# Optimization experiments

Hardware: AMD Instinct MI355X
Metric: run time of the kernel (lower is better)

## Reference

```python
import jax, jax.numpy as jnp
import numpy as np

B = 256        # graphs per batch
NPG = 256      # nodes per graph (uniform -> to_dense_batch is a reshape, mask = ones)
NTOT = B * NPG
E = 1_048_576
F_IN = 64
HID = 128
HEADS = 5
K1, K2 = 32, 8
MEMH = 100
NCLS = 12
TAU = 1.0
EPS = 1e-8


def setup_inputs() -> dict:
    key = jax.random.key(0)
    ks = jax.random.split(key, 24)
    f32 = jnp.float32
    def nrm(k, shape, s=0.05):
        return jax.random.normal(k, shape, f32) * s
    inp = {
        "x": jax.random.normal(ks[0], (NTOT, F_IN), f32),
        "edge_index": jax.random.randint(ks[1], (2, E), 0, NTOT, jnp.int32),
        "batch": jnp.repeat(jnp.arange(B, dtype=jnp.int32), NPG),
        # GraphConv q0 (num_feats -> hidden): lin_rel (bias) + lin_root (no bias)
        "W_rel0": nrm(ks[2], (F_IN, HID)), "b_rel0": jnp.zeros((HID,), f32),
        "W_root0": nrm(ks[3], (F_IN, HID)),
        # GraphConv q1 (hidden -> hidden)
        "W_rel1": nrm(ks[4], (HID, HID)), "b_rel1": jnp.zeros((HID,), f32),
        "W_root1": nrm(ks[5], (HID, HID)),
        # BatchNorm1d affine params
        "bn_gamma": jnp.ones((HID,), f32), "bn_beta": jnp.zeros((HID,), f32),
        # MemConv layer 0: keys ~ U[0,1) as torch.rand, conv1x1 [heads], lin F->MEMH
        "keys0": jax.random.uniform(ks[6], (HEADS, K1, HID), f32),
        "convw0": nrm(ks[7], (HEADS,), 0.2),
        "lin_W0": nrm(ks[8], (HID, MEMH)), "lin_b0": jnp.zeros((MEMH,), f32),
        # MemConv layer 1 (num_features = mem_hidden_dim)
        "keys1": jax.random.uniform(ks[9], (HEADS, K2, MEMH), f32),
        "convw1": nrm(ks[10], (HEADS,), 0.2),
        "lin_W1": nrm(ks[11], (MEMH, MEMH)), "lin_b1": jnp.zeros((MEMH,), f32),
        # MLP head
        "mlp_W1": nrm(ks[12], (MEMH, 50)), "mlp_b1": jnp.zeros((50,), f32),
        "mlp_W2": nrm(ks[13], (50, NCLS)), "mlp_b2": jnp.zeros((NCLS,), f32),
    }
    return inp


def _graph_conv(x, src, dst, W_rel, b_rel, W_root):
    # PyG GraphConv, aggr='add': out_i = lin_rel(sum_{j in N(i)} x_j) + lin_root(x_i)
    msg = x[src]                                            # [E, F] gather
    aggr = jax.ops.segment_sum(msg, dst, num_segments=NTOT)  # [N, F] scatter-add
    return aggr @ W_rel + b_rel + x @ W_root


def _kl_reg(C):
    P = C ** 2
    cn = C.sum(axis=-2, keepdims=True) + EPS
    P = P / cn
    pn = P.sum(axis=-1, keepdims=True) + EPS
    P = P / pn
    return 100.0 * (P * (jnp.log(P + EPS) - jnp.log(C + EPS))).sum()


def _mem_conv(Q, keys, conv_w, lin_W, lin_b, mask):
    # Q: [B, N, F]; keys: [H, K, F]; mask: [B, N] or None
    # pairwise L2 distance via norm expansion (same math as the broadcast-diff)
    qsq = (Q * Q).sum(-1)                                   # [B, N]
    ksq = (keys * keys).sum(-1)                             # [H, K]
    qk = jnp.einsum('bnf,hkf->bhnk', Q, keys)               # [B, H, N, K]
    d2 = qsq[:, None, :, None] + ksq[None, :, None, :] - 2.0 * qk
    C = jnp.sqrt(jnp.maximum(d2, 1e-12))
    if mask is not None:
        ext = mask[:, None, :, None]                        # [B,1,N,1]
        C = C * ext
    # gmn kernel: student-t style normalization over keys
    C = (1.0 + C * C / TAU) ** (-(0.5 * TAU + 0.5))
    C = C / C.sum(axis=-1, keepdims=True)
    if mask is not None:
        C = C * ext
    # conv1x1 over heads (no bias) then squeeze head dim
    C = jnp.einsum('h,bhnk->bnk', conv_w, C)
    C = jax.nn.softmax(C, axis=-1)                          # [B, N, K]
    if mask is not None:
        C = C * mask[:, :, None]
    kl = _kl_reg(C)
    V = jnp.einsum('bnk,bnf->bkf', C, Q)                    # [B, K, F]
    out = jax.nn.leaky_relu(V @ lin_W + lin_b)              # slope 0.01 (torch default)
    return out, kl


def reference(x, edge_index, batch, W_rel0, b_rel0, W_root0, W_rel1, b_rel1,
              W_root1, bn_gamma, bn_beta, keys0, convw0, lin_W0, lin_b0,
              keys1, convw1, lin_W1, lin_b1, mlp_W1, mlp_b1, mlp_W2, mlp_b2):
    src, dst = edge_index[0], edge_index[1]
    q = jax.nn.relu(_graph_conv(x, src, dst, W_rel0, b_rel0, W_root0))
    q = jax.nn.relu(_graph_conv(q, src, dst, W_rel1, b_rel1, W_root1))
    # BatchNorm1d over all (padded-)node rows, training stats, eps=1e-5
    mu = q.mean(axis=0)
    var = ((q - mu) ** 2).mean(axis=0)
    q = (q - mu) * jax.lax.rsqrt(var + 1e-5) * bn_gamma + bn_beta
    Q = q.reshape(B, NPG, HID)                              # to_dense_batch (uniform graphs)
    mask = jnp.ones((B, NPG), jnp.float32)
    q1, kl1 = _mem_conv(Q, keys0, convw0, lin_W0, lin_b0, mask)
    q2, kl2 = _mem_conv(q1, keys1, convw1, lin_W1, lin_b1, None)
    h = q2.mean(axis=-2)                                    # [B, MEMH]
    yh = jax.nn.leaky_relu(h @ mlp_W1 + mlp_b1) @ mlp_W2 + mlp_b2
    return yh, (kl1 + kl2) / NTOT
```

## Files before the change

kernel.cpp:

```cpp
#include <hip/hip_runtime.h>
#include <hip/hip_bf16.h>

#define NTOT   65536
#define NEDGE  1048576
#define HEADS  5
#define K1     32
#define K2     8
#define MEMH   100
#define EPSF   1e-8f

#define OFF_DEG     0x0000000
#define OFF_CURSOR  0x0040000
#define OFF_WT1     0x0040000
#define OFF_WT2     0x0050000
#define OFF_OFFS    0x0080000
#define OFF_BNSUM   0x00C0000
#define OFF_BNSQ    0x00C0400
#define OFF_SCALE   0x00C0800
#define OFF_SHIFT   0x00C0A00
#define OFF_KSQ0    0x00C0C00
#define OFF_KSQ1    0x00C0E80
#define OFF_KL      0x00C0F40
#define OFF_FLAG    0x00C0F60
#define OFF_W       0x00C1000
#define OFF_K0B     0x0128000
#define OFF_CN      0x0134000
#define OFF_BH      0x013C000
#define OFF_EBASE   0x013C400
#define OFF_BCUR    0x013C800
#define OFF_CSR     0x0140000
#define OFF_A       0x0540000
#define OFF_AH128   0x0540000
#define OFF_AL128   0x1540000
#define OFF_AH64    0x0540000
#define OFF_AL64    0x0D40000
#define OFF_B       0x2540000
#define OFF_EBUF    0x2540000
#define OFF_QH      0x2540000
#define OFF_QL      0x3540000
#define OFF_C       0x4540000
#define OFF_XH      0x4540000
#define OFF_XL      0x4D40000
#define OFF_CG      0x4540000
#define OFF_V       0x4D40000
#define OFF_MQ1     0x5140000
#define OFF_MQ2     0x5460000

#define W_WREL0  0
#define W_BREL0  8192
#define W_WROOT0 8320
#define W_WREL1  16512
#define W_BREL1  32896
#define W_WROOT1 33024
#define W_GAMMA  49408
#define W_BETA   49536
#define W_KEYS0  49664
#define W_CONVW0 70144
#define W_LINW0  70149
#define W_LINB0  82949
#define W_KEYS1  83049
#define W_CONVW1 87049
#define W_LINW1  87054
#define W_LINB1  97054
#define W_MLPW1  97154
#define W_MLPB1  102154
#define W_MLPW2  102204
#define W_MLPB2  102804
#define W_TOTAL  102816

typedef __attribute__((ext_vector_type(8))) short  bf16x8;
typedef __attribute__((ext_vector_type(4))) float  f32x4;

__device__ __forceinline__ float bf2f(unsigned short u){
  union { unsigned int i; float f; } v; v.i = ((unsigned int)u) << 16; return v.f;
}
__device__ __forceinline__ unsigned short f2bf(float f){
  union { float f; unsigned int i; } v; v.f = f;
  unsigned int r = (v.i + 0x7FFFu + ((v.i >> 16) & 1u)) >> 16;
  return (unsigned short)r;
}

__device__ const int g_seg[21] = {0,8192,8320,16512,32896,33024,49408,49536,49664,
                                  70144,70149,82949,83049,87049,87054,97054,97154,
                                  102154,102204,102804,102816};
struct WPtrs { const void* p[20]; };

__global__ void k_detect(const unsigned short* __restrict__ xr, int* flag){
  int t = threadIdx.x & 63;
  unsigned short u = xr[2*t];
  int e = (u >> 7) & 0xFF;
  bool plaus = (u != 0) && (e >= 115) && (e <= 135);
  unsigned long long m = __ballot(plaus);
  if(t == 0) flag[0] = (__popcll(m) >= 48) ? 1 : 0;
}

__global__ __launch_bounds__(256) void k_cvtx(const void* __restrict__ xin,
                                              const int* __restrict__ flag,
                                              unsigned short* __restrict__ xH,
                                              unsigned short* __restrict__ xL){
  int i = blockIdx.x*256 + threadIdx.x;
  float v;
  if(flag[0]) v = bf2f(((const unsigned short*)xin)[i]);
  else        v = ((const float*)xin)[i];
  unsigned short h = f2bf(v);
  xH[i] = h;
  xL[i] = f2bf(v - bf2f(h));
}

__global__ __launch_bounds__(256) void k_cvtw(WPtrs wp, const int* __restrict__ flag,
                                              float* __restrict__ wout){
  int i = blockIdx.x*256 + threadIdx.x;
  if(i >= W_TOTAL) return;
  int s = 0;
  #pragma unroll
  for(int k=0;k<20;k++) if(i >= g_seg[k+1]) s = k+1;
  int j = i - g_seg[s];
  const void* src = wp.p[s];
  wout[i] = flag[0] ? bf2f(((const unsigned short*)src)[j]) : ((const float*)src)[j];
}

__global__ __launch_bounds__(256) void k_cvtaux(const float* __restrict__ W,
                                                unsigned short* __restrict__ k0b,
                                                unsigned short* __restrict__ wt1,
                                                unsigned short* __restrict__ wt2){
  int i = blockIdx.x*256 + threadIdx.x;
  if(i < HEADS*K1*128) k0b[i] = f2bf(W[W_KEYS0 + i]);
  if(i < 128*64){
    int col = i>>6, k = i&63;
    float wr = W[W_WREL0  + k*128 + col];
    float wo = W[W_WROOT0 + k*128 + col];
    unsigned short rh = f2bf(wr), oh = f2bf(wo);
    wt1[i]         = rh;
    wt1[ 8192 + i] = f2bf(wr - bf2f(rh));
    wt1[16384 + i] = oh;
    wt1[24576 + i] = f2bf(wo - bf2f(oh));
  }
  if(i < 128*128){
    int col = i>>7, k = i&127;
    float wr = W[W_WREL1  + k*128 + col];
    float wo = W[W_WROOT1 + k*128 + col];
    unsigned short rh = f2bf(wr), oh = f2bf(wo);
    wt2[i]         = rh;
    wt2[16384 + i] = f2bf(wr - bf2f(rh));
    wt2[32768 + i] = oh;
    wt2[49152 + i] = f2bf(wo - bf2f(oh));
  }
}

__global__ __launch_bounds__(256) void k_init(unsigned long long* bnsum,
                                              unsigned long long* bnsq, float* kl, float* cn,
                                              int* bhist){
  int i = blockIdx.x*256 + threadIdx.x;
  if(i < 128){ bnsum[i]=0ULL; bnsq[i]=0ULL; }
  if(i < 2) kl[i]=0.f;
  if(i < 256*32) cn[i]=0.f;
  if(i < 256) bhist[i]=0;
}

__global__ __launch_bounds__(256) void k_bin1(const int* __restrict__ dst, int* bhist){
  __shared__ int hist[256];
  const int t = threadIdx.x;
  hist[t] = 0; __syncthreads();
  const int e0 = blockIdx.x*4096 + t;
  #pragma unroll 4
  for(int j=0;j<16;j++) atomicAdd(&hist[dst[e0 + j*256] >> 8], 1);
  __syncthreads();
  if(hist[t]) atomicAdd(&bhist[t], hist[t]);
}

__global__ __launch_bounds__(256) void k_bscan(const int* __restrict__ bhist,
                                               int* ebase, int* bcur){
  __shared__ int ts[256];
  const int t = threadIdx.x;
  ts[t] = bhist[t]; __syncthreads();
  for(int off=1; off<256; off<<=1){
    int v = (t>=off) ? ts[t-off] : 0;
    __syncthreads(); ts[t] += v; __syncthreads();
  }
  int ex = (t==0) ? 0 : ts[t-1];
  ebase[t] = ex; bcur[t] = ex;
}

__global__ __launch_bounds__(256) void k_bin2(const int* __restrict__ src, const int* __restrict__ dst,
                                              int* bcur, unsigned int* __restrict__ ebuf){
  __shared__ int hist[256], lofs[256], lcur[256], gbase[256];
  __shared__ unsigned int sbuf[4096];
  const int t = threadIdx.x;
  hist[t] = 0; __syncthreads();
  const int e0 = blockIdx.x*4096;
  unsigned int pair[16]; int bk[16];
  #pragma unroll 4
  for(int j=0;j<16;j++){
    int e = e0 + t + j*256;
    int s = src[e], d = dst[e];
    pair[j] = (((unsigned)d)<<16) | (unsigned)s;
    bk[j] = d>>8;
    atomicAdd(&hist[bk[j]], 1);
  }
  __syncthreads();
  lcur[t] = hist[t]; __syncthreads();
  for(int off=1; off<256; off<<=1){
    int v = (t>=off) ? lcur[t-off] : 0;
    __syncthreads(); lcur[t] += v; __syncthreads();
  }
  lofs[t] = (t==0) ? 0 : lcur[t-1];
  __syncthreads();
  lcur[t] = lofs[t];
  if(hist[t]) gbase[t] = atomicAdd(&bcur[t], hist[t]);
  __syncthreads();
  #pragma unroll 4
  for(int j=0;j<16;j++){
    int p = atomicAdd(&lcur[bk[j]], 1);
    sbuf[p] = pair[j];
  }
  __syncthreads();
  const int n = hist[t], lo = lofs[t], go = gbase[t];
  for(int i=0;i<n;i++) ebuf[go + i] = sbuf[lo + i];
}

__global__ __launch_bounds__(256) void k_fine(const unsigned int* __restrict__ ebuf,
                                              const int* __restrict__ ebase,
                                              unsigned short* __restrict__ csr,
                                              int* __restrict__ deg, int* __restrict__ offs){
  __shared__ int ldeg[256], lofs[256], lcur[256];
  __shared__ unsigned int led[8192];
  __shared__ unsigned short lcsr[8192];
  const int b = blockIdx.x, t = threadIdx.x;
  const int base = ebase[b];
  const int n = ((b==255) ? NEDGE : ebase[b+1]) - base;
  ldeg[t] = 0; __syncthreads();
  for(int i=t; i<n; i+=256){
    unsigned int p = ebuf[base+i];
    led[i] = p;
    atomicAdd(&ldeg[(p>>16)&255], 1);
  }
  __syncthreads();
  lcur[t] = ldeg[t]; __syncthreads();
  for(int off=1; off<256; off<<=1){
    int v = (t>=off) ? lcur[t-off] : 0;
    __syncthreads(); lcur[t] += v; __syncthreads();
  }
  lofs[t] = (t==0) ? 0 : lcur[t-1];
  __syncthreads();
  lcur[t] = lofs[t];
  __syncthreads();
  for(int i=t; i<n; i+=256){
    unsigned int p = led[i];
    int d = (p>>16)&255;
    int pos = atomicAdd(&lcur[d], 1);
    lcsr[pos] = (unsigned short)(p & 0xFFFF);
  }
  __syncthreads();
  for(int i=t; i<n; i+=256) csr[base+i] = lcsr[i];
  deg[b*256 + t]  = ldeg[t];
  offs[b*256 + t] = base + lofs[t];
}

__global__ __launch_bounds__(256) void k_aggr64(const unsigned short* __restrict__ xH,
                                                const int* __restrict__ offs, const int* __restrict__ deg,
                                                const unsigned short* __restrict__ csr,
                                                unsigned short* __restrict__ aH,
                                                unsigned short* __restrict__ aL){
  const int wid  = (blockIdx.x*256 + threadIdx.x) >> 6;
  const int lane = threadIdx.x & 63;
  const int sub = lane >> 4, fl = lane & 15;
  const int beg = offs[wid], n = deg[wid];
  float4 acc = {0.f,0.f,0.f,0.f};
  int i = 0;
  for(; i+32 <= n; i += 32){
    int s[8];
    #pragma unroll
    for(int j=0;j<8;j++) s[j] = csr[beg + i + 4*j + sub];
    #pragma unroll
    for(int j=0;j<8;j++){
      ushort4 u = *(const ushort4*)(xH + (size_t)s[j]*64 + fl*4);
      acc.x += bf2f(u.x); acc.y += bf2f(u.y); acc.z += bf2f(u.z); acc.w += bf2f(u.w);
    }
  }
  for(; i < n; i += 4){
    if(i + sub < n){
      int s = csr[beg + i + sub];
      ushort4 u = *(const ushort4*)(xH + (size_t)s*64 + fl*4);
      acc.x += bf2f(u.x); acc.y += bf2f(u.y); acc.z += bf2f(u.z); acc.w += bf2f(u.w);
    }
  }
  acc.x += __shfl_xor(acc.x, 16); acc.y += __shfl_xor(acc.y, 16);
  acc.z += __shfl_xor(acc.z, 16); acc.w += __shfl_xor(acc.w, 16);
  acc.x += __shfl_xor(acc.x, 32); acc.y += __shfl_xor(acc.y, 32);
  acc.z += __shfl_xor(acc.z, 32); acc.w += __shfl_xor(acc.w, 32);
  if(sub == 0){
    ushort4 h, l;
    h.x=f2bf(acc.x); l.x=f2bf(acc.x-bf2f(h.x));
    h.y=f2bf(acc.y); l.y=f2bf(acc.y-bf2f(h.y));
    h.z=f2bf(acc.z); l.z=f2bf(acc.z-bf2f(h.z));
    h.w=f2bf(acc.w); l.w=f2bf(acc.w-bf2f(h.w));
    *(ushort4*)(aH + (size_t)wid*64 + fl*4) = h;
    *(ushort4*)(aL + (size_t)wid*64 + fl*4) = l;
  }
}

__global__ __launch_bounds__(256) void k_aggr128(const unsigned short* __restrict__ qH,
                                                 const int* __restrict__ offs, const int* __restrict__ deg,
                                                 const unsigned short* __restrict__ csr,
                                                 unsigned short* __restrict__ aH,
                                                 unsigned short* __restrict__ aL){
  const int wid  = (blockIdx.x*256 + threadIdx.x) >> 6;
  const int lane = threadIdx.x & 63;
  const int sub = lane >> 5, fl = lane & 31;
  const int beg = offs[wid], n = deg[wid];
  float4 acc = {0.f,0.f,0.f,0.f};
  int i = 0;
  for(; i+16 <= n; i += 16){
    int s[8];
    #pragma unroll
    for(int j=0;j<8;j++) s[j] = csr[beg + i + 2*j + sub];
    #pragma unroll
    for(int j=0;j<8;j++){
      ushort4 u = *(const ushort4*)(qH + (size_t)s[j]*128 + fl*4);
      acc.x += bf2f(u.x); acc.y += bf2f(u.y); acc.z += bf2f(u.z); acc.w += bf2f(u.w);
    }
  }
  for(; i < n; i += 2){
    if(i + sub < n){
      int s = csr[beg + i + sub];
      ushort4 u = *(const ushort4*)(qH + (size_t)s*128 + fl*4);
      acc.x += bf2f(u.x); acc.y += bf2f(u.y); acc.z += bf2f(u.z); acc.w += bf2f(u.w);
    }
  }
  acc.x += __shfl_xor(acc.x, 32); acc.y += __shfl_xor(acc.y, 32);
  acc.z += __shfl_xor(acc.z, 32); acc.w += __shfl_xor(acc.w, 32);
  if(sub == 0){
    ushort4 h, l;
    h.x=f2bf(acc.x); l.x=f2bf(acc.x-bf2f(h.x));
    h.y=f2bf(acc.y); l.y=f2bf(acc.y-bf2f(h.y));
    h.z=f2bf(acc.z); l.z=f2bf(acc.z-bf2f(h.z));
    h.w=f2bf(acc.w); l.w=f2bf(acc.w-bf2f(h.w));
    *(ushort4*)(aH + (size_t)wid*128 + fl*4) = h;
    *(ushort4*)(aL + (size_t)wid*128 + fl*4) = l;
  }
}

template<int KD>
__global__ __launch_bounds__(256) void k_ling(const unsigned short* __restrict__ AH,
                                              const unsigned short* __restrict__ AL,
                                              const unsigned short* XH,
                                              const unsigned short* XL,
                                              const unsigned short* __restrict__ WT,
                                              const float* __restrict__ W, int bofs,
                                              unsigned short* outH,
                                              unsigned short* outL){
  constexpr int NK = KD/32;
  const int t = threadIdx.x;
  const int wv = t>>6, lane = t&63, quad = lane>>4, m = lane&15;
  const int rbase = blockIdx.x*128;
  const int c0 = (wv*2)*16 + m;
  const int c1 = (wv*2+1)*16 + m;

  bf16x8 BrH0[NK], BrL0[NK], BoH0[NK], BoL0[NK];
  bf16x8 BrH1[NK], BrL1[NK], BoH1[NK], BoL1[NK];
  #pragma unroll
  for(int ks=0; ks<NK; ks++){
    const size_t o0 = (size_t)c0*KD + ks*32 + quad*8;
    const size_t o1 = (size_t)c1*KD + ks*32 + quad*8;
    BrH0[ks] = *(const bf16x8*)(WT + o0);
    BrL0[ks] = *(const bf16x8*)(WT + 128*KD + o0);
    BoH0[ks] = *(const bf16x8*)(WT + 256*KD + o0);
    BoL0[ks] = *(const bf16x8*)(WT + 384*KD + o0);
    BrH1[ks] = *(const bf16x8*)(WT + o1);
    BrL1[ks] = *(const bf16x8*)(WT + 128*KD + o1);
    BoH1[ks] = *(const bf16x8*)(WT + 256*KD + o1);
    BoL1[ks] = *(const bf16x8*)(WT + 384*KD + o1);
  }
  const float b0 = W[bofs + c0];
  const float b1 = W[bofs + c1];

  for(int rt=0; rt<8; rt++){
    const int r0 = rbase + rt*16;
    bf16x8 fah[NK], fal[NK], fxh[NK], fxl[NK];
    #pragma unroll
    for(int ks=0; ks<NK; ks++){
      const size_t o = (size_t)(r0+m)*KD + ks*32 + quad*8;
      fah[ks] = *(const bf16x8*)(AH + o);
      fal[ks] = *(const bf16x8*)(AL + o);
      fxh[ks] = *(const bf16x8*)(XH + o);
      fxl[ks] = *(const bf16x8*)(XL + o);
    }
    f32x4 a0 = {0.f,0.f,0.f,0.f}, a1 = {0.f,0.f,0.f,0.f};
    #pragma unroll
    for(int ks=0; ks<NK; ks++){
      a0 = __builtin_amdgcn_mfma_f32_16x16x32_bf16(fah[ks], BrH0[ks], a0, 0,0,0);
      a1 = __builtin_amdgcn_mfma_f32_16x16x32_bf16(fah[ks], BrH1[ks], a1, 0,0,0);
      a0 = __builtin_amdgcn_mfma_f32_16x16x32_bf16(fal[ks], BrH0[ks], a0, 0,0,0);
      a1 = __builtin_amdgcn_mfma_f32_16x16x32_bf16(fal[ks], BrH1[ks], a1, 0,0,0);
      a0 = __builtin_amdgcn_mfma_f32_16x16x32_bf16(fah[ks], BrL0[ks], a0, 0,0,0);
      a1 = __builtin_amdgcn_mfma_f32_16x16x32_bf16(fah[ks], BrL1[ks], a1, 0,0,0);
      a0 = __builtin_amdgcn_mfma_f32_16x16x32_bf16(fxh[ks], BoH0[ks], a0, 0,0,0);
      a1 = __builtin_amdgcn_mfma_f32_16x16x32_bf16(fxh[ks], BoH1[ks], a1, 0,0,0);
      a0 = __builtin_amdgcn_mfma_f32_16x16x32_bf16(fxl[ks], BoH0[ks], a0, 0,0,0);
      a1 = __builtin_amdgcn_mfma_f32_16x16x32_bf16(fxl[ks], BoH1[ks], a1, 0,0,0);
      a0 = __builtin_amdgcn_mfma_f32_16x16x32_bf16(fxh[ks], BoL0[ks], a0, 0,0,0);
      a1 = __builtin_amdgcn_mfma_f32_16x16x32_bf16(fxh[ks], BoL1[ks], a1, 0,0,0);
    }
    __syncthreads();
    #pragma unroll
    for(int i=0;i<4;i++){
      const size_t orow = (size_t)(r0 + quad*4 + i)*128;
      float v0 = fmaxf(a0[i] + b0, 0.f);
      unsigned short h0 = f2bf(v0);
      outH[orow + c0] = h0;
      outL[orow + c0] = f2bf(v0 - bf2f(h0));
      float v1 = fmaxf(a1[i] + b1, 0.f);
      unsigned short h1 = f2bf(v1);
      outH[orow + c1] = h1;
      outL[orow + c1] = f2bf(v1 - bf2f(h1));
    }
  }
}

__global__ __launch_bounds__(128) void k_bnstats(const unsigned short* __restrict__ qH,
                                                 const unsigned short* __restrict__ qL,
                                                 double* bnsum, double* bnsq){
  const int j = threadIdx.x;
  const int r0 = blockIdx.x*128;
  float s=0.f, s2=0.f;
  for(int r=0;r<128;r++){
    size_t o = (size_t)(r0+r)*128 + j;
    float v = bf2f(qH[o]) + bf2f(qL[o]);
    s += v; s2 += v*v;
  }
  atomicAdd(&bnsum[j], (double)s);
  atomicAdd(&bnsq[j], (double)s2);
}

__global__ __launch_bounds__(256) void k_bnfin(const double* __restrict__ bnsum, const double* __restrict__ bnsq,
                                               const float* __restrict__ W,
                                               float* scale, float* shift, float* ksq0, float* ksq1){
  const int t = threadIdx.x;
  if(t < 128){
    double mu  = bnsum[t] / (double)NTOT;
    double var = bnsq[t] / (double)NTOT - mu*mu;
    if(var < 0.0) var = 0.0;
    float sc = W[W_GAMMA + t] * rsqrtf((float)var + 1e-5f);
    scale[t] = sc;
    shift[t] = W[W_BETA + t] - (float)mu * sc;
  }
  if(t < HEADS*K1){
    float s=0.f;
    for(int f=0;f<128;f++){ float v = W[W_KEYS0 + t*128 + f]; s += v*v; }
    ksq0[t] = s;
  }
  if(t < HEADS*K2){
    float s=0.f;
    for(int f=0;f<100;f++){ float v = W[W_KEYS1 + t*100 + f]; s += v*v; }
    ksq1[t] = s;
  }
}

__global__ __launch_bounds__(256) void k_memA(
    const unsigned short* __restrict__ qH, const unsigned short* __restrict__ qL,
    const float* __restrict__ scale, const float* __restrict__ shift,
    const unsigned short* __restrict__ k0b,
    const float* __restrict__ W, const float* __restrict__ ksq,
    float* __restrict__ Cg, float* __restrict__ cn)
{
  __shared__ unsigned short Qb[64*136];
  __shared__ float qkL[160*68];
  __shared__ float wsumL[64*36];
  __shared__ float qsqL[64];
  __shared__ float rsL[64*6];
  const int bid = blockIdx.x;
  const int r0 = bid*64;
  const int t = threadIdx.x;
  const int wv = t>>6, lane = t&63, quad = lane>>4, m = lane&15;

  for(int idx=t; idx<64*32; idx+=256){
    int r = idx>>5, c4 = (idx&31)*4;
    size_t o = (size_t)(r0+r)*128 + c4;
    ushort4 uh = *(const ushort4*)(qH + o);
    ushort4 ul = *(const ushort4*)(qL + o);
    float4 s = *(const float4*)(scale + c4);
    float4 h = *(const float4*)(shift + c4);
    ushort4 ob;
    ob.x = f2bf((bf2f(uh.x)+bf2f(ul.x))*s.x + h.x);
    ob.y = f2bf((bf2f(uh.y)+bf2f(ul.y))*s.y + h.y);
    ob.z = f2bf((bf2f(uh.z)+bf2f(ul.z))*s.z + h.z);
    ob.w = f2bf((bf2f(uh.w)+bf2f(ul.w))*s.w + h.w);
    *(ushort4*)(Qb + r*136 + c4) = ob;
  }
  __syncthreads();

  {
    bf16x8 a[4];
    #pragma unroll
// ... 28 lines not shown
      if(h < HEADS){
        float rs = 0.f;
        for(int k=0;k<32;k++){
          float d2 = q2 + ksq[h*32+k] - 2.f*qkL[(h*32+k)*68 + row];
          d2 = fmaxf(d2, 1e-12f);
          rs += 1.f/(1.f+d2);
        }
        rsL[row*6+h] = W[W_CONVW0+h]/fmaxf(rs,1e-20f);
      }
    }
  }
  __syncthreads();

  {
    int row = t & 63, kq = t >> 6;
    float q2 = qsqL[row];
    for(int kk=0; kk<8; kk++){
      int k = kq*8+kk;
      float wsum = 0.f;
      #pragma unroll
      for(int h=0;h<HEADS;h++){
        float d2 = q2 + ksq[h*32+k] - 2.f*qkL[(h*32+k)*68 + row];
        d2 = fmaxf(d2, 1e-12f);
        wsum += rsL[row*6+h]/(1.f+d2);
      }
      wsumL[row*36+k] = wsum;
    }
  }
  __syncthreads();

  if(t < 64){
    float mx = -1e30f;
    #pragma unroll
    for(int k=0;k<32;k++) mx = fmaxf(mx, wsumL[t*36+k]);
    float cv[32]; float se = 0.f;
    #pragma unroll
    for(int k=0;k<32;k++){ float e = __expf(wsumL[t*36+k]-mx); cv[k]=e; se+=e; }
    float inv = 1.f/se;
    #pragma unroll
    for(int k=0;k<32;k++){ cv[k]*=inv; wsumL[t*36+k]=cv[k]; }
    float4* dst = (float4*)(Cg + (size_t)(r0+t)*32);
    #pragma unroll
    for(int k4=0;k4<8;k4++)
      dst[k4] = (float4){cv[k4*4],cv[k4*4+1],cv[k4*4+2],cv[k4*4+3]};
  }
  __syncthreads();
  if(t < 32){
    float s = 0.f;
    for(int r=0;r<64;r++) s += wsumL[r*36+t];
    atomicAdd(&cn[(bid>>2)*32 + t], s);
  }
}

__global__ __launch_bounds__(256) void k_memB(const float* __restrict__ Cg,
                                              const float* __restrict__ cn,
                                              float* __restrict__ klacc){
  __shared__ float cn_s[32];
  __shared__ float red_s[4];
  const int b = blockIdx.x, t = threadIdx.x;
  if(t < 32) cn_s[t] = cn[b*32+t] + EPSF;
  __syncthreads();
  const float* crow = Cg + ((size_t)b*256 + t)*32;
  float cv[32]; float pn = 0.f;
  #pragma unroll
  for(int k4=0;k4<8;k4++){
    float4 u = *(const float4*)(crow + k4*4);
    cv[k4*4]=u.x; cv[k4*4+1]=u.y; cv[k4*4+2]=u.z; cv[k4*4+3]=u.w;
  }
  #pragma unroll
  for(int k=0;k<32;k++) pn += cv[k]*cv[k]/cn_s[k];
  pn += EPSF;
  float acc = 0.f;
  #pragma unroll
  for(int k=0;k<32;k++){
    float P = cv[k]*cv[k]/(cn_s[k]*pn);
    acc += P*(__logf(P+EPSF) - __logf(cv[k]+EPSF));
  }
  #pragma unroll
  for(int off=32; off>0; off>>=1) acc += __shfl_down(acc, off);
  if((t&63)==0) red_s[t>>6] = acc;
  __syncthreads();
  if(t==0) atomicAdd(klacc, 100.f*(red_s[0]+red_s[1]+red_s[2]+red_s[3]));
}

__global__ __launch_bounds__(256) void k_memV(const float* __restrict__ Cg,
                                              const unsigned short* __restrict__ qH,
                                              const unsigned short* __restrict__ qL,
                                              const float* __restrict__ scale,
                                              const float* __restrict__ shift,
                                              float* __restrict__ V){
  __shared__ float Cs[256*36];
  __shared__ float Qs[256*32];
  const int b  = blockIdx.x >> 2;
  const int f0 = (blockIdx.x & 3) * 32;
  const int t = threadIdx.x;
  for(int idx=t; idx<256*8; idx+=256){
    int n = idx>>3, k4 = (idx&7)*4;
    *(float4*)(Cs + n*36 + k4) = *(const float4*)(Cg + ((size_t)b*256+n)*32 + k4);
  }
  for(int idx=t; idx<256*8; idx+=256){
    int n = idx>>3, j4 = (idx&7)*4;
    size_t o = ((size_t)b*256+n)*128 + f0 + j4;
    ushort4 uh = *(const ushort4*)(qH + o);
    ushort4 ul = *(const ushort4*)(qL + o);
    float4 s = *(const float4*)(scale + f0 + j4);
    float4 h = *(const float4*)(shift + f0 + j4);
    *(float4*)(Qs + n*32 + j4) = (float4){
      (bf2f(uh.x)+bf2f(ul.x))*s.x + h.x,
      (bf2f(uh.y)+bf2f(ul.y))*s.y + h.y,
      (bf2f(uh.z)+bf2f(ul.z))*s.z + h.z,
      (bf2f(uh.w)+bf2f(ul.w))*s.w + h.w};
  }
  __syncthreads();
  const int k = t & 31, fg = t >> 5;
  float v0=0.f,v1=0.f,v2=0.f,v3=0.f;
  for(int n=0;n<256;n++){
    float c = Cs[n*36+k];
    float4 q = *(const float4*)(Qs + n*32 + fg*4);
    v0 += c*q.x; v1 += c*q.y; v2 += c*q.z; v3 += c*q.w;
  }
  *(float4*)(V + ((size_t)b*32 + k)*128 + f0 + fg*4) = (float4){v0,v1,v2,v3};
}

__global__ __launch_bounds__(256) void k_memL(const float* __restrict__ V,
                                              const float* __restrict__ W,
                                              float* __restrict__ mq1){
  __shared__ float Vs[32*132];
  const int b = blockIdx.x, t = threadIdx.x;
  for(int idx=t; idx<32*32; idx+=256){
    int k = idx>>5, j4 = (idx&31)*4;
    *(float4*)(Vs + k*132 + j4) = *(const float4*)(V + ((size_t)b*32+k)*128 + j4);
  }
  __syncthreads();
  for(int idx=t; idx<K1*MEMH; idx+=256){
    int k = idx/100, mc = idx - k*100;
    float a = W[W_LINB0 + mc];
    for(int f=0; f<128; f++) a += Vs[k*132+f]*W[W_LINW0 + f*100 + mc];
    mq1[(size_t)(b*32+k)*100 + mc] = (a>0.f) ? a : 0.01f*a;
  }
}

__global__ __launch_bounds__(256) void k_memconv1(
    const float* __restrict__ mq1, const float* __restrict__ W,
    const float* __restrict__ ksq, float* __restrict__ mq2, float* __restrict__ klacc)
{
  __shared__ float Qs[32*104];
  __shared__ float Ks[40*100];
  __shared__ float QKs[32*40];
// ... 88 lines not shown
    mq2[(size_t)b*800 + idx] = (a>0.f) ? a : 0.01f*a;
  }
}

__global__ __launch_bounds__(128) void k_final(const float* __restrict__ mq2,
                                               const float* __restrict__ W,
                                               const int* __restrict__ flag,
                                               const float* __restrict__ kl,
                                               void* __restrict__ out){
  __shared__ float h_s[100];
  __shared__ float hid_s[50];
  const int b = blockIdx.x, t = threadIdx.x;
  if(t < 100){
    float s=0.f;
    #pragma unroll
    for(int k=0;k<8;k++) s += mq2[(size_t)b*800 + k*100 + t];
    h_s[t] = s*0.125f;
  }
  __syncthreads();
  if(t < 50){
    float a = W[W_MLPB1 + t];
    for(int f=0;f<100;f++) a += h_s[f]*W[W_MLPW1 + f*50 + t];
    hid_s[t] = (a>0.f) ? a : 0.01f*a;
  }
  __syncthreads();
  if(t < 12){
    float a = W[W_MLPB2 + t];
    #pragma unroll
    for(int j=0;j<50;j++) a += hid_s[j]*W[W_MLPW2 + j*12 + t];
    if(flag[0]) ((__hip_bfloat16*)out)[b*12+t] = __float2bfloat16(a);
    else        ((float*)out)[b*12+t] = a;
  }
  if(b==0 && t==64){
    float v = (kl[0]+kl[1]) * (1.f/65536.f);
    if(flag[0]) ((__hip_bfloat16*)out)[3072] = __float2bfloat16(v);
    else        ((float*)out)[3072] = v;
  }
}

extern "C" void kernel_launch(void* const* d_in, const int* in_sizes, int n_in,
                              void* d_out, int out_size, void* d_ws, size_t ws_size,
                              hipStream_t stream) {
  (void)in_sizes; (void)n_in; (void)out_size; (void)ws_size;
  const void* x   = d_in[0];
  const int*  ei  = (const int*)d_in[1];
  const int* src = ei;
  const int* dst = ei + NEDGE;

  WPtrs wp;
  for(int i=0;i<20;i++) wp.p[i] = d_in[3+i];

  char* w = (char*)d_ws;
  int*    deg    = (int*)   (w + OFF_DEG);
  int*    offs   = (int*)   (w + OFF_OFFS);
  double* bnsum  = (double*)(w + OFF_BNSUM);
  double* bnsq   = (double*)(w + OFF_BNSQ);
  float*  scale  = (float*) (w + OFF_SCALE);
  float*  shift  = (float*) (w + OFF_SHIFT);
  float*  ksq0   = (float*) (w + OFF_KSQ0);
  float*  ksq1   = (float*) (w + OFF_KSQ1);
  float*  kl     = (float*) (w + OFF_KL);
  int*    flag   = (int*)   (w + OFF_FLAG);
  float*  Wc     = (float*) (w + OFF_W);
  unsigned short* k0b = (unsigned short*)(w + OFF_K0B);
  unsigned short* wt1 = (unsigned short*)(w + OFF_WT1);
  unsigned short* wt2 = (unsigned short*)(w + OFF_WT2);
  float*  cn     = (float*) (w + OFF_CN);
  int*    bhist  = (int*)   (w + OFF_BH);
  int*    ebase  = (int*)   (w + OFF_EBASE);
  int*    bcur   = (int*)   (w + OFF_BCUR);
  unsigned short* csr = (unsigned short*)(w + OFF_CSR);
  unsigned int*   ebuf = (unsigned int*)(w + OFF_EBUF);
  unsigned short* agH64  = (unsigned short*)(w + OFF_AH64);
  unsigned short* agL64  = (unsigned short*)(w + OFF_AL64);
  unsigned short* agH128 = (unsigned short*)(w + OFF_AH128);
  unsigned short* agL128 = (unsigned short*)(w + OFF_AL128);
  unsigned short* qvH    = (unsigned short*)(w + OFF_QH);
  unsigned short* qvL    = (unsigned short*)(w + OFF_QL);
  unsigned short* xcH    = (unsigned short*)(w + OFF_XH);
  unsigned short* xcL    = (unsigned short*)(w + OFF_XL);
  float*  Cg     = (float*) (w + OFF_CG);
  float*  Vbuf   = (float*) (w + OFF_V);
  float*  mq1    = (float*) (w + OFF_MQ1);
  float*  mq2    = (float*) (w + OFF_MQ2);

  unsigned short* qbnH = qvH;
  unsigned short* qbnL = qvL;

  k_detect <<<1,      64, 0, stream>>>((const unsigned short*)x, flag);
  k_init   <<<32,    256, 0, stream>>>((unsigned long long*)bnsum, (unsigned long long*)bnsq, kl, cn, bhist);
  k_bin1   <<<256,   256, 0, stream>>>(dst, bhist);
  k_bscan  <<<1,     256, 0, stream>>>(bhist, ebase, bcur);
  k_bin2   <<<256,   256, 0, stream>>>(src, dst, bcur, ebuf);
  k_fine   <<<256,   256, 0, stream>>>(ebuf, ebase, csr, deg, offs);
  k_cvtx   <<<16384, 256, 0, stream>>>(x, flag, xcH, xcL);
  k_cvtw   <<<402,   256, 0, stream>>>(wp, flag, Wc);
  k_cvtaux <<<80,    256, 0, stream>>>(Wc, k0b, wt1, wt2);
  k_aggr64 <<<16384, 256, 0, stream>>>(xcH, offs, deg, csr, agH64, agL64);
  k_ling<64> <<<512, 256, 0, stream>>>(agH64, agL64, xcH, xcL, wt1, Wc, W_BREL0, qvH, qvL);
  k_aggr128<<<16384, 256, 0, stream>>>(qvH, offs, deg, csr, agH128, agL128);
  k_ling<128><<<512, 256, 0, stream>>>(agH128, agL128, qvH, qvL, wt2, Wc, W_BREL1, qbnH, qbnL);
  k_bnstats<<<512,   128, 0, stream>>>(qbnH, qbnL, bnsum, bnsq);
  k_bnfin  <<<1,     256, 0, stream>>>(bnsum, bnsq, Wc, scale, shift, ksq0, ksq1);
  k_memA   <<<1024,  256, 0, stream>>>(qbnH, qbnL, scale, shift, k0b, Wc, ksq0, Cg, cn);
  k_memB   <<<256,   256, 0, stream>>>(Cg, cn, kl);
  k_memV   <<<1024,  256, 0, stream>>>(Cg, qbnH, qbnL, scale, shift, Vbuf);
  k_memL   <<<256,   256, 0, stream>>>(Vbuf, Wc, mq1);
  k_memconv1<<<256,  256, 0, stream>>>(mq1, Wc, ksq1, mq2, kl+1);
  k_final  <<<256,   128, 0, stream>>>(mq2, Wc, flag, kl, d_out);
}
```

Measured before the change: 479.1 us.

## Merge setup kernels, widen aggregation loads, fuse BN stats into GEMM

Several small kernels are merged: detect, init and bin1 become k_pre, which writes per-block histograms reduced in bscan instead of using atomics. cvtaux is folded into cvtw, memB into memV, and the BN statistics are accumulated inside the second GEMM epilogue, which removes a full pass over q. The neighbour-aggregation kernels switch from 4-wide to 8-wide bf16 loads, so fewer lanes cover each feature row and more edges run in parallel per wave. BN sums now use float atomics instead of double, which changes precision and makes accumulation order nondeterministic.

```diff
diff --git a/kernel.cpp b/kernel.cpp
--- a/kernel.cpp
+++ b/kernel.cpp
@@ -10,6 +10,7 @@
 #define EPSF   1e-8f
 
 #define OFF_DEG     0x0000000
+#define OFF_BH2     0x0000000
 #define OFF_CURSOR  0x0040000
 #define OFF_WT1     0x0040000
 #define OFF_WT2     0x0050000
@@ -25,7 +26,6 @@
 #define OFF_W       0x00C1000
 #define OFF_K0B     0x0128000
 #define OFF_CN      0x0134000
-#define OFF_BH      0x013C000
 #define OFF_EBASE   0x013C400
 #define OFF_BCUR    0x013C800
 #define OFF_CSR     0x0140000
@@ -85,94 +85,43 @@
                                   102154,102204,102804,102816};
 struct WPtrs { const void* p[20]; };
 
-__global__ void k_detect(const unsigned short* __restrict__ xr, int* flag){
-  int t = threadIdx.x & 63;
-  unsigned short u = xr[2*t];
-  int e = (u >> 7) & 0xFF;
-  bool plaus = (u != 0) && (e >= 115) && (e <= 135);
-  unsigned long long m = __ballot(plaus);
-  if(t == 0) flag[0] = (__popcll(m) >= 48) ? 1 : 0;
-}
-
-__global__ __launch_bounds__(256) void k_cvtx(const void* __restrict__ xin,
-                                              const int* __restrict__ flag,
-                                              unsigned short* __restrict__ xH,
-                                              unsigned short* __restrict__ xL){
-  int i = blockIdx.x*256 + threadIdx.x;
-  float v;
-  if(flag[0]) v = bf2f(((const unsigned short*)xin)[i]);
-  else        v = ((const float*)xin)[i];
-  unsigned short h = f2bf(v);
-  xH[i] = h;
-  xL[i] = f2bf(v - bf2f(h));
-}
-
-__global__ __launch_bounds__(256) void k_cvtw(WPtrs wp, const int* __restrict__ flag,
-                                              float* __restrict__ wout){
-  int i = blockIdx.x*256 + threadIdx.x;
-  if(i >= W_TOTAL) return;
-  int s = 0;
-  #pragma unroll
-  for(int k=0;k<20;k++) if(i >= g_seg[k+1]) s = k+1;
-  int j = i - g_seg[s];
-  const void* src = wp.p[s];
-  wout[i] = flag[0] ? bf2f(((const unsigned short*)src)[j]) : ((const float*)src)[j];
-}
-
-__global__ __launch_bounds__(256) void k_cvtaux(const float* __restrict__ W,
-                                                unsigned short* __restrict__ k0b,
-                                                unsigned short* __restrict__ wt1,
-                                                unsigned short* __restrict__ wt2){
-  int i = blockIdx.x*256 + threadIdx.x;
-  if(i < HEADS*K1*128) k0b[i] = f2bf(W[W_KEYS0 + i]);
-  if(i < 128*64){
-    int col = i>>6, k = i&63;
-    float wr = W[W_WREL0  + k*128 + col];
-    float wo = W[W_WROOT0 + k*128 + col];
-    unsigned short rh = f2bf(wr), oh = f2bf(wo);
-    wt1[i]         = rh;
-    wt1[ 8192 + i] = f2bf(wr - bf2f(rh));
-    wt1[16384 + i] = oh;
-    wt1[24576 + i] = f2bf(wo - bf2f(oh));
-  }
-  if(i < 128*128){
-    int col = i>>7, k = i&127;
-    float wr = W[W_WREL1  + k*128 + col];
-    float wo = W[W_WROOT1 + k*128 + col];
-    unsigned short rh = f2bf(wr), oh = f2bf(wo);
-    wt2[i]         = rh;
-    wt2[16384 + i] = f2bf(wr - bf2f(rh));
-    wt2[32768 + i] = oh;
-    wt2[49152 + i] = f2bf(wo - bf2f(oh));
-  }
-}
-
-__global__ __launch_bounds__(256) void k_init(unsigned long long* bnsum,
-                                              unsigned long long* bnsq, float* kl, float* cn,
-                                              int* bhist){
-  int i = blockIdx.x*256 + threadIdx.x;
-  if(i < 128){ bnsum[i]=0ULL; bnsq[i]=0ULL; }
-  if(i < 2) kl[i]=0.f;
-  if(i < 256*32) cn[i]=0.f;
-  if(i < 256) bhist[i]=0;
-}
-
-__global__ __launch_bounds__(256) void k_bin1(const int* __restrict__ dst, int* bhist){
+__device__ __forceinline__ float rdw(const void* p, int j, int flag){
+  return flag ? bf2f(((const unsigned short*)p)[j]) : ((const float*)p)[j];
+}
+
+__global__ __launch_bounds__(256) void k_pre(const unsigned short* __restrict__ xr,
+                                             const int* __restrict__ dst,
+                                             int* flag, float* bnsum, float* bnsq,
+                                             float* kl, float* cn, int* bh2){
   __shared__ int hist[256];
-  const int t = threadIdx.x;
+  const int b = blockIdx.x, t = threadIdx.x;
   hist[t] = 0; __syncthreads();
-  const int e0 = blockIdx.x*4096 + t;
+  const int e0 = b*4096 + t;
   #pragma unroll 4
   for(int j=0;j<16;j++) atomicAdd(&hist[dst[e0 + j*256] >> 8], 1);
   __syncthreads();
-  if(hist[t]) atomicAdd(&bhist[t], hist[t]);
-}
-
-__global__ __launch_bounds__(256) void k_bscan(const int* __restrict__ bhist,
+  bh2[b*256 + t] = hist[t];
+  if(b == 0){
+    if(t < 64){
+      unsigned short u = xr[2*t];
+      int e = (u >> 7) & 0xFF;
+      bool plaus = (u != 0) && (e >= 115) && (e <= 135);
+      unsigned long long m = __ballot(plaus);
+      if(t == 0) flag[0] = (__popcll(m) >= 48) ? 1 : 0;
+    }
+    if(t < 128){ bnsum[t]=0.f; bnsq[t]=0.f; }
+    if(t < 2) kl[t]=0.f;
+  }
+  if(b < 32) cn[b*256 + t] = 0.f;
+}
+
+__global__ __launch_bounds__(256) void k_bscan(const int* __restrict__ bh2,
                                                int* ebase, int* bcur){
   __shared__ int ts[256];
   const int t = threadIdx.x;
-  ts[t] = bhist[t]; __syncthreads();
+  int s = 0;
+  for(int b=0;b<256;b++) s += bh2[b*256 + t];
+  ts[t] = s; __syncthreads();
   for(int off=1; off<256; off<<=1){
     int v = (t>=off) ? ts[t-off] : 0;
     __syncthreads(); ts[t] += v; __syncthreads();
@@ -256,6 +205,56 @@
   offs[b*256 + t] = base + lofs[t];
 }
 
+__global__ __launch_bounds__(256) void k_cvtx(const void* __restrict__ xin,
+                                              const int* __restrict__ flag,
+                                              unsigned short* __restrict__ xH,
+                                              unsigned short* __restrict__ xL){
+  int i = blockIdx.x*256 + threadIdx.x;
+  float v = rdw(xin, i, flag[0]);
+  unsigned short h = f2bf(v);
+  xH[i] = h;
+  xL[i] = f2bf(v - bf2f(h));
+}
+
+__global__ __launch_bounds__(256) void k_cvtw(WPtrs wp, const int* __restrict__ flag,
+                                              float* __restrict__ wout,
+                                              unsigned short* __restrict__ k0b,
+                                              unsigned short* __restrict__ wt1,
+                                              unsigned short* __restrict__ wt2){
+  const int fl = flag[0];
+  if(blockIdx.x < 402){
+    int i = blockIdx.x*256 + threadIdx.x;
+    if(i >= W_TOTAL) return;
+    int s = 0;
+    #pragma unroll
+    for(int k=0;k<20;k++) if(i >= g_seg[k+1]) s = k+1;
+    wout[i] = rdw(wp.p[s], i - g_seg[s], fl);
+  } else {
+    int i = (blockIdx.x-402)*256 + threadIdx.x;
+    if(i < HEADS*K1*128) k0b[i] = f2bf(rdw(wp.p[8], i, fl));
+    if(i < 128*64){
+      int col = i>>6, k = i&63;
+      float wr = rdw(wp.p[0], k*128 + col, fl);
+      float wo = rdw(wp.p[2], k*128 + col, fl);
+      unsigned short rh = f2bf(wr), oh = f2bf(wo);
+      wt1[i]         = rh;
+      wt1[ 8192 + i] = f2bf(wr - bf2f(rh));
+      wt1[16384 + i] = oh;
+      wt1[24576 + i] = f2bf(wo - bf2f(oh));
+    }
+    if(i < 128*128){
+      int col = i>>7, k = i&127;
+      float wr = rdw(wp.p[3], k*128 + col, fl);
+      float wo = rdw(wp.p[5], k*128 + col, fl);
+      unsigned short rh = f2bf(wr), oh = f2bf(wo);
+      wt2[i]         = rh;
+      wt2[16384 + i] = f2bf(wr - bf2f(rh));
+      wt2[32768 + i] = oh;
+      wt2[49152 + i] = f2bf(wo - bf2f(oh));
+    }
+  }
+}
+
 __global__ __launch_bounds__(256) void k_aggr64(const unsigned short* __restrict__ xH,
                                                 const int* __restrict__ offs, const int* __restrict__ deg,
                                                 const unsigned short* __restrict__ csr,
@@ -263,39 +262,51 @@
                                                 unsigned short* __restrict__ aL){
   const int wid  = (blockIdx.x*256 + threadIdx.x) >> 6;
   const int lane = threadIdx.x & 63;
-  const int sub = lane >> 4, fl = lane & 15;
+  const int sub = lane >> 3, fl = lane & 7;
   const int beg = offs[wid], n = deg[wid];
-  float4 acc = {0.f,0.f,0.f,0.f};
+  float acc[8];
+  #pragma unroll
+  for(int e=0;e<8;e++) acc[e]=0.f;
   int i = 0;
-  for(; i+32 <= n; i += 32){
+  for(; i+64 <= n; i += 64){
     int s[8];
     #pragma unroll
-    for(int j=0;j<8;j++) s[j] = csr[beg + i + 4*j + sub];
+    for(int j=0;j<8;j++) s[j] = csr[beg + i + 8*j + sub];
     #pragma unroll
     for(int j=0;j<8;j++){
-      ushort4 u = *(const ushort4*)(xH + (size_t)s[j]*64 + fl*4);
-      acc.x += bf2f(u.x); acc.y += bf2f(u.y); acc.z += bf2f(u.z); acc.w += bf2f(u.w);
-    }
-  }
-  for(; i < n; i += 4){
+      bf16x8 u = *(const bf16x8*)(xH + (size_t)s[j]*64 + fl*8);
+      #pragma unroll
+      for(int e=0;e<8;e++) acc[e] += bf2f((unsigned short)u[e]);
+    }
+  }
+  for(; i < n; i += 8){
     if(i + sub < n){
       int s = csr[beg + i + sub];
-      ushort4 u = *(const ushort4*)(xH + (size_t)s*64 + fl*4);
-      acc.x += bf2f(u.x); acc.y += bf2f(u.y); acc.z += bf2f(u.z); acc.w += bf2f(u.w);
-    }
-  }
-  acc.x += __shfl_xor(acc.x, 16); acc.y += __shfl_xor(acc.y, 16);
-  acc.z += __shfl_xor(acc.z, 16); acc.w += __shfl_xor(acc.w, 16);
-  acc.x += __shfl_xor(acc.x, 32); acc.y += __shfl_xor(acc.y, 32);
-  acc.z += __shfl_xor(acc.z, 32); acc.w += __shfl_xor(acc.w, 32);
+      bf16x8 u = *(const bf16x8*)(xH + (size_t)s*64 + fl*8);
+      #pragma unroll
+      for(int e=0;e<8;e++) acc[e] += bf2f((unsigned short)u[e]);
+    }
+  }
+  #pragma unroll
+  for(int e=0;e<8;e++){
+    acc[e] += __shfl_xor(acc[e], 8);
+    acc[e] += __shfl_xor(acc[e], 16);
+    acc[e] += __shfl_xor(acc[e], 32);
+  }
   if(sub == 0){
-    ushort4 h, l;
-    h.x=f2bf(acc.x); l.x=f2bf(acc.x-bf2f(h.x));
-    h.y=f2bf(acc.y); l.y=f2bf(acc.y-bf2f(h.y));
-    h.z=f2bf(acc.z); l.z=f2bf(acc.z-bf2f(h.z));
-    h.w=f2bf(acc.w); l.w=f2bf(acc.w-bf2f(h.w));
-    *(ushort4*)(aH + (size_t)wid*64 + fl*4) = h;
-    *(ushort4*)(aL + (size_t)wid*64 + fl*4) = l;
+    ushort4 h0,h1,l0,l1;
+    h0.x=f2bf(acc[0]); l0.x=f2bf(acc[0]-bf2f(h0.x));
+    h0.y=f2bf(acc[1]); l0.y=f2bf(acc[1]-bf2f(h0.y));
+    h0.z=f2bf(acc[2]); l0.z=f2bf(acc[2]-bf2f(h0.z));
+    h0.w=f2bf(acc[3]); l0.w=f2bf(acc[3]-bf2f(h0.w));
+    h1.x=f2bf(acc[4]); l1.x=f2bf(acc[4]-bf2f(h1.x));
+    h1.y=f2bf(acc[5]); l1.y=f2bf(acc[5]-bf2f(h1.y));
+    h1.z=f2bf(acc[6]); l1.z=f2bf(acc[6]-bf2f(h1.z));
+    h1.w=f2bf(acc[7]); l1.w=f2bf(acc[7]-bf2f(h1.w));
+    *(ushort4*)(aH + (size_t)wid*64 + fl*8)     = h0;
+    *(ushort4*)(aH + (size_t)wid*64 + fl*8 + 4) = h1;
+    *(ushort4*)(aL + (size_t)wid*64 + fl*8)     = l0;
+    *(ushort4*)(aL + (size_t)wid*64 + fl*8 + 4) = l1;
   }
 }
 
@@ -306,41 +317,54 @@
                                                  unsigned short* __restrict__ aL){
   const int wid  = (blockIdx.x*256 + threadIdx.x) >> 6;
   const int lane = threadIdx.x & 63;
-  const int sub = lane >> 5, fl = lane & 31;
+  const int sub = lane >> 4, fl = lane & 15;
   const int beg = offs[wid], n = deg[wid];
-  float4 acc = {0.f,0.f,0.f,0.f};
+  float acc[8];
+  #pragma unroll
+  for(int e=0;e<8;e++) acc[e]=0.f;
   int i = 0;
-  for(; i+16 <= n; i += 16){
+  for(; i+32 <= n; i += 32){
     int s[8];
     #pragma unroll
-    for(int j=0;j<8;j++) s[j] = csr[beg + i + 2*j + sub];
+    for(int j=0;j<8;j++) s[j] = csr[beg + i + 4*j + sub];
     #pragma unroll
     for(int j=0;j<8;j++){
-      ushort4 u = *(const ushort4*)(qH + (size_t)s[j]*128 + fl*4);
-      acc.x += bf2f(u.x); acc.y += bf2f(u.y); acc.z += bf2f(u.z); acc.w += bf2f(u.w);
-    }
-  }
-  for(; i < n; i += 2){
+      bf16x8 u = *(const bf16x8*)(qH + (size_t)s[j]*128 + fl*8);
+      #pragma unroll
+      for(int e=0;e<8;e++) acc[e] += bf2f((unsigned short)u[e]);
+    }
+  }
+  for(; i < n; i += 4){
     if(i + sub < n){
       int s = csr[beg + i + sub];
-      ushort4 u = *(const ushort4*)(qH + (size_t)s*128 + fl*4);
-      acc.x += bf2f(u.x); acc.y += bf2f(u.y); acc.z += bf2f(u.z); acc.w += bf2f(u.w);
-    }
-  }
-  acc.x += __shfl_xor(acc.x, 32); acc.y += __shfl_xor(acc.y, 32);
-  acc.z += __shfl_xor(acc.z, 32); acc.w += __shfl_xor(acc.w, 32);
+      bf16x8 u = *(const bf16x8*)(qH + (size_t)s*128 + fl*8);
+      #pragma unroll
+      for(int e=0;e<8;e++) acc[e] += bf2f((unsigned short)u[e]);
+    }
+  }
+  #pragma unroll
+  for(int e=0;e<8;e++){
+    acc[e] += __shfl_xor(acc[e], 16);
+    acc[e] += __shfl_xor(acc[e], 32);
+  }
   if(sub == 0){
-    ushort4 h, l;
-    h.x=f2bf(acc.x); l.x=f2bf(acc.x-bf2f(h.x));
-    h.y=f2bf(acc.y); l.y=f2bf(acc.y-bf2f(h.y));
-    h.z=f2bf(acc.z); l.z=f2bf(acc.z-bf2f(h.z));
-    h.w=f2bf(acc.w); l.w=f2bf(acc.w-bf2f(h.w));
-    *(ushort4*)(aH + (size_t)wid*128 + fl*4) = h;
-    *(ushort4*)(aL + (size_t)wid*128 + fl*4) = l;
-  }
-}
-
-template<int KD>
+    ushort4 h0,h1,l0,l1;
+    h0.x=f2bf(acc[0]); l0.x=f2bf(acc[0]-bf2f(h0.x));
+    h0.y=f2bf(acc[1]); l0.y=f2bf(acc[1]-bf2f(h0.y));
+    h0.z=f2bf(acc[2]); l0.z=f2bf(acc[2]-bf2f(h0.z));
+    h0.w=f2bf(acc[3]); l0.w=f2bf(acc[3]-bf2f(h0.w));
+    h1.x=f2bf(acc[4]); l1.x=f2bf(acc[4]-bf2f(h1.x));
+    h1.y=f2bf(acc[5]); l1.y=f2bf(acc[5]-bf2f(h1.y));
+    h1.z=f2bf(acc[6]); l1.z=f2bf(acc[6]-bf2f(h1.z));
+    h1.w=f2bf(acc[7]); l1.w=f2bf(acc[7]-bf2f(h1.w));
+    *(ushort4*)(aH + (size_t)wid*128 + fl*8)     = h0;
+    *(ushort4*)(aH + (size_t)wid*128 + fl*8 + 4) = h1;
+    *(ushort4*)(aL + (size_t)wid*128 + fl*8)     = l0;
+    *(ushort4*)(aL + (size_t)wid*128 + fl*8 + 4) = l1;
+  }
+}
+
+template<int KD, bool STATS>
 __global__ __launch_bounds__(256) void k_ling(const unsigned short* __restrict__ AH,
                                               const unsigned short* __restrict__ AL,
                                               const unsigned short* XH,
@@ -348,7 +372,8 @@
                                               const unsigned short* __restrict__ WT,
                                               const float* __restrict__ W, int bofs,
                                               unsigned short* outH,
-                                              unsigned short* outL){
+                                              unsigned short* outL,
+                                              float* bnsum, float* bnsq){
   constexpr int NK = KD/32;
   const int t = threadIdx.x;
   const int wv = t>>6, lane = t&63, quad = lane>>4, m = lane&15;
@@ -373,6 +398,7 @@
   }
   const float b0 = W[bofs + c0];
   const float b1 = W[bofs + c1];
+  float s1a=0.f, s2a=0.f, s1b=0.f, s2b=0.f;
 
   for(int rt=0; rt<8; rt++){
     const int r0 = rbase + rt*16;
@@ -413,32 +439,31 @@
       unsigned short h1 = f2bf(v1);
       outH[orow + c1] = h1;
       outL[orow + c1] = f2bf(v1 - bf2f(h1));
-    }
-  }
-}
-
-__global__ __launch_bounds__(128) void k_bnstats(const unsigned short* __restrict__ qH,
-                                                 const unsigned short* __restrict__ qL,
-                                                 double* bnsum, double* bnsq){
-  const int j = threadIdx.x;
-  const int r0 = blockIdx.x*128;
-  float s=0.f, s2=0.f;
-  for(int r=0;r<128;r++){
-    size_t o = (size_t)(r0+r)*128 + j;
-    float v = bf2f(qH[o]) + bf2f(qL[o]);
-    s += v; s2 += v*v;
-  }
-  atomicAdd(&bnsum[j], (double)s);
-  atomicAdd(&bnsq[j], (double)s2);
-}
-
-__global__ __launch_bounds__(256) void k_bnfin(const double* __restrict__ bnsum, const double* __restrict__ bnsq,
+      if(STATS){
+        s1a += v0; s2a += v0*v0;
+        s1b += v1; s2b += v1*v1;
+      }
+    }
+  }
+  if(STATS){
+    s1a += __shfl_xor(s1a,16); s1a += __shfl_xor(s1a,32);
+    s2a += __shfl_xor(s2a,16); s2a += __shfl_xor(s2a,32);
+    s1b += __shfl_xor(s1b,16); s1b += __shfl_xor(s1b,32);
+    s2b += __shfl_xor(s2b,16); s2b += __shfl_xor(s2b,32);
+    if(quad == 0){
+      atomicAdd(&bnsum[c0], s1a); atomicAdd(&bnsq[c0], s2a);
+      atomicAdd(&bnsum[c1], s1b); atomicAdd(&bnsq[c1], s2b);
+    }
+  }
+}
+
+__global__ __launch_bounds__(256) void k_bnfin(const float* __restrict__ bnsum, const float* __restrict__ bnsq,
                                                const float* __restrict__ W,
                                                float* scale, float* shift, float* ksq0, float* ksq1){
   const int t = threadIdx.x;
   if(t < 128){
-    double mu  = bnsum[t] / (double)NTOT;
-    double var = bnsq[t] / (double)NTOT - mu*mu;
+    double mu  = (double)bnsum[t] / (double)NTOT;
+    double var = (double)bnsq[t] / (double)NTOT - mu*mu;
     if(var < 0.0) var = 0.0;
     float sc = W[W_GAMMA + t] * rsqrtf((float)var + 1e-5f);
     scale[t] = sc;
@@ -573,48 +598,46 @@
   }
 }
 
-__global__ __launch_bounds__(256) void k_memB(const float* __restrict__ Cg,
-                                              const float* __restrict__ cn,
-                                              float* __restrict__ klacc){
-  __shared__ float cn_s[32];
-  __shared__ float red_s[4];
-  const int b = blockIdx.x, t = threadIdx.x;
-  if(t < 32) cn_s[t] = cn[b*32+t] + EPSF;
-  __syncthreads();
-  const float* crow = Cg + ((size_t)b*256 + t)*32;
-  float cv[32]; float pn = 0.f;
-  #pragma unroll
-  for(int k4=0;k4<8;k4++){
-    float4 u = *(const float4*)(crow + k4*4);
-    cv[k4*4]=u.x; cv[k4*4+1]=u.y; cv[k4*4+2]=u.z; cv[k4*4+3]=u.w;
-  }
-  #pragma unroll
-  for(int k=0;k<32;k++) pn += cv[k]*cv[k]/cn_s[k];
-  pn += EPSF;
-  float acc = 0.f;
-  #pragma unroll
-  for(int k=0;k<32;k++){
-    float P = cv[k]*cv[k]/(cn_s[k]*pn);
-    acc += P*(__logf(P+EPSF) - __logf(cv[k]+EPSF));
-  }
-  #pragma unroll
-  for(int off=32; off>0; off>>=1) acc += __shfl_down(acc, off);
-  if((t&63)==0) red_s[t>>6] = acc;
-  __syncthreads();
-  if(t==0) atomicAdd(klacc, 100.f*(red_s[0]+red_s[1]+red_s[2]+red_s[3]));
-}
-
-__global__ __launch_bounds__(256) void k_memV(const float* __restrict__ Cg,
-                                              const unsigned short* __restrict__ qH,
-                                              const unsigned short* __restrict__ qL,
-                                              const float* __restrict__ scale,
-                                              const float* __restrict__ shift,
-                                              float* __restrict__ V){
+__global__ __launch_bounds__(256) void k_memVB(const float* __restrict__ Cg,
+                                               const unsigned short* __restrict__ qH,
+                                               const unsigned short* __restrict__ qL,
+                                               const float* __restrict__ scale,
+                                               const float* __restrict__ shift,
+                                               const float* __restrict__ cn,
+                                               float* __restrict__ V,
+                                               float* __restrict__ klacc){
   __shared__ float Cs[256*36];
   __shared__ float Qs[256*32];
+  const int t = threadIdx.x;
+  if(blockIdx.x >= 1024){
+    const int b = blockIdx.x - 1024;
+    if(t < 32) Cs[t] = cn[b*32+t] + EPSF;
+    __syncthreads();
+    const float* crow = Cg + ((size_t)b*256 + t)*32;
+    float cv[32]; float pn = 0.f;
+    #pragma unroll
+    for(int k4=0;k4<8;k4++){
+      float4 u = *(const float4*)(crow + k4*4);
+      cv[k4*4]=u.x; cv[k4*4+1]=u.y; cv[k4*4+2]=u.z; cv[k4*4+3]=u.w;
+    }
+    #pragma unroll
+    for(int k=0;k<32;k++) pn += cv[k]*cv[k]/Cs[k];
+    pn += EPSF;
+    float acc = 0.f;
+    #pragma unroll
+    for(int k=0;k<32;k++){
+      float P = cv[k]*cv[k]/(Cs[k]*pn);
+      acc += P*(__logf(P+EPSF) - __logf(cv[k]+EPSF));
+    }
+    #pragma unroll
+    for(int off=32; off>0; off>>=1) acc += __shfl_down(acc, off);
+    if((t&63)==0) Qs[t>>6] = acc;
+    __syncthreads();
+    if(t==0) atomicAdd(klacc, 100.f*(Qs[0]+Qs[1]+Qs[2]+Qs[3]));
+    return;
+  }
   const int b  = blockIdx.x >> 2;
   const int f0 = (blockIdx.x & 3) * 32;
-  const int t = threadIdx.x;
   for(int idx=t; idx<256*8; idx+=256){
     int n = idx>>3, k4 = (idx&7)*4;
     *(float4*)(Cs + n*36 + k4) = *(const float4*)(Cg + ((size_t)b*256+n)*32 + k4);
@@ -809,9 +832,10 @@
 
   char* w = (char*)d_ws;
   int*    deg    = (int*)   (w + OFF_DEG);
+  int*    bh2    = (int*)   (w + OFF_BH2);
   int*    offs   = (int*)   (w + OFF_OFFS);
-  double* bnsum  = (double*)(w + OFF_BNSUM);
-  double* bnsq   = (double*)(w + OFF_BNSQ);
+  float*  bnsum  = (float*) (w + OFF_BNSUM);
+  float*  bnsq   = (float*) (w + OFF_BNSQ);
   float*  scale  = (float*) (w + OFF_SCALE);
   float*  shift  = (float*) (w + OFF_SHIFT);
   float*  ksq0   = (float*) (w + OFF_KSQ0);
@@ -823,7 +847,6 @@
   unsigned short* wt1 = (unsigned short*)(w + OFF_WT1);
   unsigned short* wt2 = (unsigned short*)(w + OFF_WT2);
   float*  cn     = (float*) (w + OFF_CN);
-  int*    bhist  = (int*)   (w + OFF_BH);
   int*    ebase  = (int*)   (w + OFF_EBASE);
   int*    bcur   = (int*)   (w + OFF_BCUR);
   unsigned short* csr = (unsigned short*)(w + OFF_CSR);
@@ -844,24 +867,19 @@
   unsigned short* qbnH = qvH;
   unsigned short* qbnL = qvL;
 
-  k_detect <<<1,      64, 0, stream>>>((const unsigned short*)x, flag);
-  k_init   <<<32,    256, 0, stream>>>((unsigned long long*)bnsum, (unsigned long long*)bnsq, kl, cn, bhist);
-  k_bin1   <<<256,   256, 0, stream>>>(dst, bhist);
-  k_bscan  <<<1,     256, 0, stream>>>(bhist, ebase, bcur);
+  k_pre    <<<256,   256, 0, stream>>>((const unsigned short*)x, dst, flag, bnsum, bnsq, kl, cn, bh2);
+  k_bscan  <<<1,     256, 0, stream>>>(bh2, ebase, bcur);
   k_bin2   <<<256,   256, 0, stream>>>(src, dst, bcur, ebuf);
   k_fine   <<<256,   256, 0, stream>>>(ebuf, ebase, csr, deg, offs);
   k_cvtx   <<<16384, 256, 0, stream>>>(x, flag, xcH, xcL);
-  k_cvtw   <<<402,   256, 0, stream>>>(wp, flag, Wc);
-  k_cvtaux <<<80,    256, 0, stream>>>(Wc, k0b, wt1, wt2);
+  k_cvtw   <<<482,   256, 0, stream>>>(wp, flag, Wc, k0b, wt1, wt2);
   k_aggr64 <<<16384, 256, 0, stream>>>(xcH, offs, deg, csr, agH64, agL64);
-  k_ling<64> <<<512, 256, 0, stream>>>(agH64, agL64, xcH, xcL, wt1, Wc, W_BREL0, qvH, qvL);
+  k_ling<64,false> <<<512, 256, 0, stream>>>(agH64, agL64, xcH, xcL, wt1, Wc, W_BREL0, qvH, qvL, bnsum, bnsq);
   k_aggr128<<<16384, 256, 0, stream>>>(qvH, offs, deg, csr, agH128, agL128);
-  k_ling<128><<<512, 256, 0, stream>>>(agH128, agL128, qvH, qvL, wt2, Wc, W_BREL1, qbnH, qbnL);
-  k_bnstats<<<512,   128, 0, stream>>>(qbnH, qbnL, bnsum, bnsq);
+  k_ling<128,true><<<512, 256, 0, stream>>>(agH128, agL128, qvH, qvL, wt2, Wc, W_BREL1, qbnH, qbnL, bnsum, bnsq);
   k_bnfin  <<<1,     256, 0, stream>>>(bnsum, bnsq, Wc, scale, shift, ksq0, ksq1);
   k_memA   <<<1024,  256, 0, stream>>>(qbnH, qbnL, scale, shift, k0b, Wc, ksq0, Cg, cn);
-  k_memB   <<<256,   256, 0, stream>>>(Cg, cn, kl);
-  k_memV   <<<1024,  256, 0, stream>>>(Cg, qbnH, qbnL, scale, shift, Vbuf);
+  k_memVB  <<<1280,  256, 0, stream>>>(Cg, qbnH, qbnL, scale, shift, cn, Vbuf, kl);
   k_memL   <<<256,   256, 0, stream>>>(Vbuf, Wc, mq1);
   k_memconv1<<<256,  256, 0, stream>>>(mq1, Wc, ksq1, mq2, kl+1);
   k_final  <<<256,   128, 0, stream>>>(mq2, Wc, flag, kl, d_out);
```

After: 457.8 us. 1.05x faster.
